# Kernel optimization log

Hardware: AMD Instinct MI355X
Metric: run time of the kernel (lower is better)

Reference implementation:

```python
import jax, jax.numpy as jnp
import numpy as np

B, N, E, K = 4, 40000, 240000, 128
C_IN, C_W, C_OUT, N_BLOCK = 6, 128, 3, 4


def setup_inputs() -> dict:
    key = jax.random.key(0)
    ks = jax.random.split(key, 20)
    s = lambda k, sh, fan: jax.random.normal(k, sh, jnp.float32) / np.sqrt(fan).astype(np.float32)
    inp = {}
    inp["x_in"] = jax.random.normal(ks[0], (B, N, C_IN), jnp.float32)
    inp["mass"] = jax.random.uniform(ks[1], (B, N), jnp.float32) + 0.1  # positive lumped mass
    inp["evals"] = jax.random.uniform(ks[2], (B, K), jnp.float32) * 10.0  # nonneg Laplacian eigenvalues
    inp["evecs"] = jax.random.normal(ks[3], (B, N, K), jnp.float32) / np.float32(np.sqrt(N))
    inp["rows"] = jax.random.randint(ks[4], (E,), 0, N, jnp.int32)
    inp["cols"] = jax.random.randint(ks[5], (E,), 0, N, jnp.int32)
    inp["gradX_vals"] = jax.random.normal(ks[6], (B, E), jnp.float32)
    inp["gradY_vals"] = jax.random.normal(ks[7], (B, E), jnp.float32)
    inp["w_first"] = s(ks[8], (C_IN, C_W), C_IN)
    inp["b_first"] = jnp.zeros((C_W,), jnp.float32)
    inp["diff_time"] = jax.random.uniform(ks[9], (N_BLOCK, C_W), jnp.float32) * 0.1 + 1e-4  # learned times, clamped positive
    inp["A_re"] = s(ks[10], (N_BLOCK, C_W, C_W), C_W)
    inp["A_im"] = s(ks[11], (N_BLOCK, C_W, C_W), C_W)
    inp["mlp_w0"] = s(ks[12], (N_BLOCK, 3 * C_W, C_W), 3 * C_W)
    inp["mlp_b0"] = jnp.zeros((N_BLOCK, C_W), jnp.float32)
    inp["mlp_w1"] = s(ks[13], (N_BLOCK, C_W, C_W), C_W)
    inp["mlp_b1"] = jnp.zeros((N_BLOCK, C_W), jnp.float32)
    inp["mlp_w2"] = s(ks[14], (N_BLOCK, C_W, C_W), C_W)
    inp["mlp_b2"] = jnp.zeros((N_BLOCK, C_W), jnp.float32)
    inp["w_last"] = s(ks[15], (C_W, C_OUT), C_W)
    inp["b_last"] = jnp.zeros((C_OUT,), jnp.float32)
    return inp


def reference(x_in, mass, evals, evecs, rows, cols, gradX_vals, gradY_vals,
              w_first, b_first, diff_time, A_re, A_im,
              mlp_w0, mlp_b0, mlp_w1, mlp_b1, mlp_w2, mlp_b2, w_last, b_last):
    def spmm(vals, x):
        # sparse [N,N] COO (shared pattern, per-sample vals) @ dense [N,C]
        return jax.ops.segment_sum(vals[:, None] * x[cols], rows, num_segments=N)

    x = x_in @ w_first + b_first  # [B,N,C_W]
    for i in range(N_BLOCK):
        # --- LearnedTimeDiffusion (spectral) ---
        x_spec = jnp.einsum('bnk,bnc->bkc', evecs, x * mass[..., None])  # [B,K,C]
        coefs = jnp.exp(-evals[:, :, None] * diff_time[i][None, None, :])  # [B,K,C]
        x_diffuse = jnp.einsum('bnk,bkc->bnc', evecs, coefs * x_spec)  # [B,N,C]
        # --- per-sample sparse gradient operators (the batched torch.mm loop) ---
        gX = jax.vmap(spmm)(gradX_vals, x_diffuse)  # [B,N,C]
        gY = jax.vmap(spmm)(gradY_vals, x_diffuse)  # [B,N,C]
        # --- SpatialGradientFeatures with learned rotations (complex multiply) ---
        Breal = gX @ A_re[i] - gY @ A_im[i]
        Bimag = gY @ A_re[i] + gX @ A_im[i]
        grad_feat = jnp.tanh(gX * Breal + gY * Bimag)  # [B,N,C]
        # --- MiniMLP + residual ---
        feat = jnp.concatenate([x, x_diffuse, grad_feat], axis=-1)  # [B,N,3C]
        h = jax.nn.relu(feat @ mlp_w0[i] + mlp_b0[i])
        h = jax.nn.relu(h @ mlp_w1[i] + mlp_b1[i])
        h = h @ mlp_w2[i] + mlp_b2[i]
        x = h + x
    return x @ w_last + b_last  # [B,N,C_OUT]
```

## Files before the change

### kernel.cpp

```cpp
#include <hip/hip_runtime.h>

#define B_ 4
#define N_ 40000
#define E_ 240000
#define NB_SCAN ((N_ + 255) / 256)

typedef unsigned short u16;
typedef unsigned int u32;
typedef __attribute__((ext_vector_type(8))) short bf16x8;
typedef __attribute__((ext_vector_type(4))) float f32x4;

__device__ __forceinline__ float b2f(u16 h) {
    u32 u = ((u32)h) << 16;
    return __uint_as_float(u);
}
__device__ __forceinline__ u16 f2b(float f) {
    u32 u = __float_as_uint(f);
    u32 r = (u + 0x7fffu + ((u >> 16) & 1u)) >> 16;
    return (u16)r;
}

__global__ __launch_bounds__(256) void first_linear_kern(
    const float* __restrict__ x_in, const float* __restrict__ w,
    const float* __restrict__ bias, u16* __restrict__ xout, int M)
{
    __shared__ float sw[6 * 128];
    __shared__ float sb[128];
    int t = threadIdx.x;
    for (int i = t; i < 768; i += 256) sw[i] = w[i];
    if (t < 128) sb[t] = bias[t];
    __syncthreads();
    int idx = blockIdx.x * 256 + t;
    int row = idx >> 4;
    int cg = (idx & 15) * 8;
    if (row >= M) return;
    const float* xr = x_in + (size_t)row * 6;
    float xv[6];
#pragma unroll
    for (int j = 0; j < 6; j++) xv[j] = xr[j];
    float acc[8];
#pragma unroll
    for (int i = 0; i < 8; i++) acc[i] = sb[cg + i];
#pragma unroll
    for (int j = 0; j < 6; j++)
#pragma unroll
        for (int i = 0; i < 8; i++) acc[i] += xv[j] * sw[j * 128 + cg + i];
    ushort4 h0, h1;
    h0.x = f2b(acc[0]); h0.y = f2b(acc[1]); h0.z = f2b(acc[2]); h0.w = f2b(acc[3]);
    h1.x = f2b(acc[4]); h1.y = f2b(acc[5]); h1.z = f2b(acc[6]); h1.w = f2b(acc[7]);
    uint4 pk;
    pk.x = (u32)h0.x | ((u32)h0.y << 16);
    pk.y = (u32)h0.z | ((u32)h0.w << 16);
    pk.z = (u32)h1.x | ((u32)h1.y << 16);
    pk.w = (u32)h1.z | ((u32)h1.w << 16);
    *(uint4*)(xout + (size_t)row * 128 + cg) = pk;
}

__global__ __launch_bounds__(256) void pack_w_kern(
    const float* __restrict__ src, u16* __restrict__ dst, int K)
{
    int i = blockIdx.z;
    src += (size_t)i * K * 128;
    dst += (size_t)i * K * 128;
    int idx = blockIdx.x * 256 + threadIdx.x;
    int n = idx / K;
    int k = idx % K;
    dst[idx] = f2b(src[(size_t)k * 128 + n]);
}

__global__ __launch_bounds__(256) void pack_rot_kern(
    const float* __restrict__ Are, const float* __restrict__ Aim,
    u16* __restrict__ WR1, u16* __restrict__ WR2)
{
    int i = blockIdx.z;
    const float* are = Are + (size_t)i * 16384;
    const float* aim = Aim + (size_t)i * 16384;
    int idx = blockIdx.x * 256 + threadIdx.x;
    int n = idx >> 8;
    int k = idx & 255;
    float v1, v2;
    if (k < 128) { float a = are[(size_t)k * 128 + n]; v1 = a; v2 = a; }
    else         { float a = aim[(size_t)(k - 128) * 128 + n]; v1 = -a; v2 = a; }
    WR1[(size_t)i * 32768 + idx] = f2b(v1);
    WR2[(size_t)i * 32768 + idx] = f2b(v2);
}

__global__ __launch_bounds__(256) void hist_kern(const int* __restrict__ rows, int* count)
{
    int e = blockIdx.x * 256 + threadIdx.x;
    if (e < E_) atomicAdd(&count[rows[e]], 1);
}

__device__ __forceinline__ int block_incl_scan_256(int v, int t)
{
    __shared__ int wsum[4];
    int lane = t & 63;
    int wid = t >> 6;
    int x = v;
#pragma unroll
    for (int off = 1; off < 64; off <<= 1) {
        int y = __shfl_up(x, off);
        if (lane >= off) x += y;
    }
    if (lane == 63) wsum[wid] = x;
    __syncthreads();
    if (t == 0) {
        int s = 0;
#pragma unroll
        for (int i = 0; i < 4; i++) { int tm = wsum[i]; wsum[i] = s; s += tm; }
    }
    __syncthreads();
    return x + wsum[wid];
}

__global__ __launch_bounds__(256) void scan1_kern(
    const int* __restrict__ count, int* __restrict__ excl_out,
    int* __restrict__ blockTotals)
{
    int t = threadIdx.x;
    int g = blockIdx.x * 256 + t;
    int v = (g < N_) ? count[g] : 0;
    int incl = block_incl_scan_256(v, t);
    if (g < N_) excl_out[g] = incl - v;
    if (t == 255) blockTotals[blockIdx.x] = incl;
}

__global__ __launch_bounds__(256) void scan2_kern(
    const int* __restrict__ blockTotals, int* __restrict__ blockOffs,
    int* __restrict__ totalOut)
{
    int t = threadIdx.x;
    int v = (t < NB_SCAN) ? blockTotals[t] : 0;
    int incl = block_incl_scan_256(v, t);
    if (t < NB_SCAN) blockOffs[t] = incl - v;
    if (t == 255) *totalOut = incl;
}

__global__ __launch_bounds__(256) void scan3_kern(
    int* __restrict__ rowptr, int* __restrict__ nextp,
    const int* __restrict__ blockOffs)
{
    int t = threadIdx.x;
    int g = blockIdx.x * 256 + t;
    if (g >= N_) return;
    int v = rowptr[g] + blockOffs[blockIdx.x];
    rowptr[g] = v;
    nextp[g] = v;
}

__global__ __launch_bounds__(256) void scatter_idx_kern(
    const int* __restrict__ rows, const int* __restrict__ cols,
    int* nextp, int* __restrict__ scols, int* __restrict__ sperm)
{
    int e = blockIdx.x * 256 + threadIdx.x;
    if (e >= E_) return;
    int r = rows[e];
    int pos = atomicAdd(&nextp[r], 1);
    scols[pos] = cols[e];
    sperm[pos] = e;
}

__global__ __launch_bounds__(256) void gather_vals_kern(
    const int* __restrict__ sperm,
    const float* __restrict__ gvx, const float* __restrict__ gvy,
    float* __restrict__ svx, float* __restrict__ svy)
{
    int pos = blockIdx.x * 256 + threadIdx.x;
    if (pos >= E_) return;
    int e = sperm[pos];
#pragma unroll
    for (int b = 0; b < B_; b++) {
        svx[(size_t)b * E_ + pos] = gvx[(size_t)b * E_ + e];
        svy[(size_t)b * E_ + pos] = gvy[(size_t)b * E_ + e];
    }
}

__global__ __launch_bounds__(256) void spmm_csr_kern(
    const int* __restrict__ rowptr, const int* __restrict__ scols,
    const float* __restrict__ svx, const float* __restrict__ svy,
    const u16* __restrict__ xd_b, u16* __restrict__ gXh, u16* __restrict__ gYh)
{
    int t = threadIdx.x;
    int r = blockIdx.x * 4 + (t >> 6);
    int c2 = (t & 63) * 2;
    int beg = rowptr[r], end = rowptr[r + 1];
    float ax0 = 0.f, ax1 = 0.f, ay0 = 0.f, ay1 = 0.f;
    int j = beg;
    for (; j + 1 < end; j += 2) {
        int ca = scols[j], cb = scols[j + 1];
        u32 xwa = *(const u32*)(xd_b + (size_t)ca * 128 + c2);
        u32 xwb = *(const u32*)(xd_b + (size_t)cb * 128 + c2);
        float vxa = svx[j], vya = svy[j];
        float vxb = svx[j + 1], vyb = svy[j + 1];
        float xa0 = b2f((u16)(xwa & 0xffffu)), xa1 = b2f((u16)(xwa >> 16));
        float xb0 = b2f((u16)(xwb & 0xffffu)), xb1 = b2f((u16)(xwb >> 16));
        ax0 += vxa * xa0; ax1 += vxa * xa1;
        ay0 += vya * xa0; ay1 += vya * xa1;
        ax0 += vxb * xb0; ax1 += vxb * xb1;
        ay0 += vyb * xb0; ay1 += vyb * xb1;
    }
    if (j < end) {
        int col = scols[j];
        u32 xw = *(const u32*)(xd_b + (size_t)col * 128 + c2);
        float x0 = b2f((u16)(xw & 0xffffu));
        float x1 = b2f((u16)(xw >> 16));
        float vx = svx[j], vy = svy[j];
        ax0 += vx * x0; ax1 += vx * x1;
        ay0 += vy * x0; ay1 += vy * x1;
    }
    u32 px = (u32)f2b(ax0) | ((u32)f2b(ax1) << 16);
    u32 py = (u32)f2b(ay0) | ((u32)f2b(ay1) << 16);
    *(u32*)(gXh + (size_t)r * 128 + c2) = px;
    *(u32*)(gYh + (size_t)r * 128 + c2) = py;
}

__global__ __launch_bounds__(256) void spec_stage1_mfma_kern(
    const u16* __restrict__ x, const float* __restrict__ mass,
    const float* __restrict__ evecs, float* __restrict__ partials)
{
    __shared__ __align__(16) u16 sEVh[128][40];
    __shared__ __align__(16) u16 sEVl[128][40];
    __shared__ __align__(16) u16 sXM[128][40];
    int b = blockIdx.y;
    int pb = blockIdx.x;
    const u16* xb = x + (size_t)b * N_ * 128;
    const float* mb = mass + (size_t)b * N_;
    const float* eb = evecs + (size_t)b * N_ * 128;
    float* dst = partials + ((size_t)b * 128 + pb) * 16384;

    int t = threadIdx.x;
    int wv = t >> 6;
    int lane = t & 63;
    int quad = lane >> 4;
    int r16 = lane & 15;
    int kb = wv * 32;
    int kc = (t & 63) * 2;
    int nh = wv;

    f32x4 acc[2][8];
#pragma unroll
    for (int i = 0; i < 2; i++)
#pragma unroll
        for (int j = 0; j < 8; j++) acc[i][j] = (f32x4){0.f, 0.f, 0.f, 0.f};

    for (int ch = pb; ch < N_ / 32; ch += 128) {
        int nbase = ch * 32 + nh * 8;
        float4 m0 = *(const float4*)(mb + nbase);
        float4 m1 = *(const float4*)(mb + nbase + 4);
        float mm[8] = {m0.x, m0.y, m0.z, m0.w, m1.x, m1.y, m1.z, m1.w};
        u32 eh0[4], eh1[4], el0[4], el1[4], xq0[4], xq1[4];
#pragma unroll
        for (int jp = 0; jp < 4; jp++) {
            eh0[jp] = 0; eh1[jp] = 0; el0[jp] = 0;
            el1[jp] = 0; xq0[jp] = 0; xq1[jp] = 0;
        }
#pragma unroll
        for (int j = 0; j < 8; j++) {
            float2 e = *(const float2*)(eb + (size_t)(nbase + j) * 128 + kc);
            u32 xw = *(const u32*)(xb + (size_t)(nbase + j) * 128 + kc);
            u16 h0 = f2b(e.x);
            u16 h1 = f2b(e.y);
            u16 l0 = f2b(e.x - b2f(h0));
            u16 l1 = f2b(e.y - b2f(h1));
            u16 q0 = f2b(b2f((u16)(xw & 0xffffu)) * mm[j]);
            u16 q1 = f2b(b2f((u16)(xw >> 16)) * mm[j]);
            int sh = (j & 1) * 16;
            int jp = j >> 1;
            eh0[jp] |= ((u32)h0) << sh; eh1[jp] |= ((u32)h1) << sh;
            el0[jp] |= ((u32)l0) << sh; el1[jp] |= ((u32)l1) << sh;
            xq0[jp] |= ((u32)q0) << sh; xq1[jp] |= ((u32)q1) << sh;
        }
        __syncthreads();
        *(uint4*)&sEVh[kc][nh * 8]     = make_uint4(eh0[0], eh0[1], eh0[2], eh0[3]);
        *(uint4*)&sEVh[kc + 1][nh * 8] = make_uint4(eh1[0], eh1[1], eh1[2], eh1[3]);
        *(uint4*)&sEVl[kc][nh * 8]     = make_uint4(el0[0], el0[1], el0[2], el0[3]);
        *(uint4*)&sEVl[kc + 1][nh * 8] = make_uint4(el1[0], el1[1], el1[2], el1[3]);
        *(uint4*)&sXM[kc][nh * 8]      = make_uint4(xq0[0], xq0[1], xq0[2], xq0[3]);
        *(uint4*)&sXM[kc + 1][nh * 8]  = make_uint4(xq1[0], xq1[1], xq1[2], xq1[3]);
        __syncthreads();

        bf16x8 ah0 = *(const bf16x8*)&sEVh[kb + r16][quad * 8];
        bf16x8 ah1 = *(const bf16x8*)&sEVh[kb + 16 + r16][quad * 8];
        bf16x8 al0 = *(const bf16x8*)&sEVl[kb + r16][quad * 8];
        bf16x8 al1 = *(const bf16x8*)&sEVl[kb + 16 + r16][quad * 8];
#pragma unroll
        for (int nt = 0; nt < 8; nt++) {
            bf16x8 bx = *(const bf16x8*)&sXM[nt * 16 + r16][quad * 8];
            acc[0][nt] = __builtin_amdgcn_mfma_f32_16x16x32_bf16(ah0, bx, acc[0][nt], 0, 0, 0);
            acc[1][nt] = __builtin_amdgcn_mfma_f32_16x16x32_bf16(ah1, bx, acc[1][nt], 0, 0, 0);
            acc[0][nt] = __builtin_amdgcn_mfma_f32_16x16x32_bf16(al0, bx, acc[0][nt], 0, 0, 0);
            acc[1][nt] = __builtin_amdgcn_mfma_f32_16x16x32_bf16(al1, bx, acc[1][nt], 0, 0, 0);
        }
    }

#pragma unroll
    for (int mt = 0; mt < 2; mt++)
#pragma unroll
        for (int nt = 0; nt < 8; nt++)
#pragma unroll
            for (int reg = 0; reg < 4; reg++) {
                int kk = kb + mt * 16 + quad * 4 + reg;
                int cc = nt * 16 + r16;
                dst[(size_t)kk * 128 + cc] = acc[mt][nt][reg];
            }
}

__global__ __launch_bounds__(128) void spec_stage2_coef_kern(
    const float* __restrict__ partials, const float* __restrict__ evals,
    const float* __restrict__ dt, u16* __restrict__ ys_t)
{
    int b = blockIdx.x >> 7;
    int k = blockIdx.x & 127;
    int c = threadIdx.x;
    const float* p = partials + (size_t)b * 128 * 16384 + (size_t)k * 128 + c;
    float s = 0.f;
#pragma unroll 8
    for (int pb = 0; pb < 128; pb++) s += p[(size_t)pb * 16384];
    float co = expf(-evals[b * 128 + k] * dt[c]);
    ys_t[((size_t)b * 128 + c) * 128 + k] = f2b(s * co);
}

template <int KK, bool AF32>
__global__ __launch_bounds__(256) void mgemm_kern(
    const void* __restrict__ A0v,
    const u16* __restrict__ Wp, u16* __restrict__ outp,
    size_t aBatch, size_t wBatch, size_t oBatch)
{
    __shared__ u16 sA[64][72];
    __shared__ u16 sB[128][72];
    int z = blockIdx.z;
    const u16* Wb = Wp + wBatch * (size_t)z;
    size_t aOff = aBatch * (size_t)z;
    size_t oOff = oBatch * (size_t)z;

    int t = threadIdx.x;
    int m0 = blockIdx.x * 64;
    int wv = t >> 6;
    int lane = t & 63;
    int quad = lane >> 4;
    int r16 = lane & 15;
    int mw = (wv & 1) * 32;
    int nw = (wv >> 1) * 64;

    f32x4 acc[2][4];
#pragma unroll
    for (int i = 0; i < 2; i++)
#pragma unroll
        for (int j = 0; j < 4; j++) acc[i][j] = (f32x4){0.f, 0.f, 0.f, 0.f};

#pragma unroll 1
    for (int kt = 0; kt < KK / 64; kt++) {
        int kbase = kt * 64;
        __syncthreads();
        if (AF32) {
            const float* Af = (const float*)A0v + aOff;
#pragma unroll
            for (int p = 0; p < 4; p++) {
                int idx = p * 256 + t;
                int row = idx >> 4;
                int seg = idx & 15;
                float4 v = *(const float4*)(Af + (size_t)(m0 + row) * 128 + kbase + seg * 4);
                ushort4 h;
                h.x = f2b(v.x); h.y = f2b(v.y); h.z = f2b(v.z); h.w = f2b(v.w);
                *(ushort4*)&sA[row][seg * 4] = h;
            }
        } else {
            const u16* Ah = (const u16*)A0v + aOff;
#pragma unroll
            for (int p = 0; p < 2; p++) {
                int idx = p * 256 + t;
                int row = idx >> 3;
                int seg = idx & 7;
                *(uint4*)&sA[row][seg * 8] =
                    *(const uint4*)(Ah + (size_t)(m0 + row) * 128 + kbase + seg * 8);
            }
        }
        {
#pragma unroll
            for (int p = 0; p < 4; p++) {
                int idx = p * 256 + t;
                int n = idx >> 3;
                int seg = idx & 7;
                *(uint4*)&sB[n][seg * 8] =
                    *(const uint4*)(Wb + (size_t)n * KK + kbase + seg * 8);
            }
        }
        __syncthreads();

#pragma unroll
        for (int ks = 0; ks < 2; ks++) {
            int ko = ks * 32 + quad * 8;
            bf16x8 a0 = *(const bf16x8*)&sA[mw + r16][ko];
            bf16x8 a1 = *(const bf16x8*)&sA[mw + 16 + r16][ko];
            bf16x8 b0 = *(const bf16x8*)&sB[nw + r16][ko];
            bf16x8 b1 = *(const bf16x8*)&sB[nw + 16 + r16][ko];
            bf16x8 b2 = *(const bf16x8*)&sB[nw + 32 + r16][ko];
            bf16x8 b3 = *(const bf16x8*)&sB[nw + 48 + r16][ko];
            acc[0][0] = __builtin_amdgcn_mfma_f32_16x16x32_bf16(a0, b0, acc[0][0], 0, 0, 0);
            acc[0][1] = __builtin_amdgcn_mfma_f32_16x16x32_bf16(a0, b1, acc[0][1], 0, 0, 0);
            acc[0][2] = __builtin_amdgcn_mfma_f32_16x16x32_bf16(a0, b2, acc[0][2], 0, 0, 0);
            acc[0][3] = __builtin_amdgcn_mfma_f32_16x16x32_bf16(a0, b3, acc[0][3], 0, 0, 0);
            acc[1][0] = __builtin_amdgcn_mfma_f32_16x16x32_bf16(a1, b0, acc[1][0], 0, 0, 0);
            acc[1][1] = __builtin_amdgcn_mfma_f32_16x16x32_bf16(a1, b1, acc[1][1], 0, 0, 0);
            acc[1][2] = __builtin_amdgcn_mfma_f32_16x16x32_bf16(a1, b2, acc[1][2], 0, 0, 0);
            acc[1][3] = __builtin_amdgcn_mfma_f32_16x16x32_bf16(a1, b3, acc[1][3], 0, 0, 0);
        }
    }

#pragma unroll
    for (int nt = 0; nt < 4; nt++) {
        int col = nw + nt * 16 + r16;
#pragma unroll
        for (int mt = 0; mt < 2; mt++) {
#pragma unroll
            for (int reg = 0; reg < 4; reg++) {
                int row = m0 + mw + mt * 16 + quad * 4 + reg;
                outp[oOff + (size_t)row * 128 + col] = f2b(acc[mt][nt][reg]);
            }
        }
    }
}

__global__ __launch_bounds__(256) void mlp_rot_fused_kern(
    const u16* __restrict__ xg, const u16* __restrict__ xdg,
    const u16* __restrict__ gXY,
    const u16* __restrict__ WR1, const u16* __restrict__ WR2,
    const u16* __restrict__ W0, const u16* __restrict__ W1, const u16* __restrict__ W2,
    const float* __restrict__ b0, const float* __restrict__ b1, const float* __restrict__ b2,
    int batch0, u16* __restrict__ outp)
{
    __shared__ u16 sGX[64][136];
    __shared__ u16 sGY[64][136];
    __shared__ u16 sB[128][72];
    __shared__ __align__(16) u16 sHbuf[9728];
    __shared__ u16 sA[64][72];
#define HV(r, c) sHbuf[(r) * 152 + (c)]
#define WV(n, c) sHbuf[(n) * 72 + (c)]

    const size_t NZ = (size_t)N_ * 128;
    int z = blockIdx.z;
    int batch = batch0 + z;
    const u16* gX = gXY + (size_t)z * 2 * NZ;
    const u16* gY = gX + NZ;
    int m0n = blockIdx.x * 64;
    size_t growBase = ((size_t)batch * N_ + m0n) * 128;

    int t = threadIdx.x;
    int wv = t >> 6;
    int lane = t & 63;
    int quad = lane >> 4;
    int r16 = lane & 15;
    int mw = (wv & 1) * 32;
    int nw = (wv >> 1) * 64;

#pragma unroll
    for (int p = 0; p < 4; p++) {
        int idx = p * 256 + t;
        int row = idx >> 4;
        int seg = idx & 15;
        *(uint4*)&sGX[row][seg * 8] = *(const uint4*)(gX + (size_t)(m0n + row) * 128 + seg * 8);
        *(uint4*)&sGY[row][seg * 8] = *(const uint4*)(gY + (size_t)(m0n + row) * 128 + seg * 8);
    }

    f32x4 accRe[2][4], accIm[2][4];
#pragma unroll
    for (int i = 0; i < 2; i++)
#pragma unroll
        for (int j = 0; j < 4; j++) {
            accRe[i][j] = (f32x4){0.f, 0.f, 0.f, 0.f};
            accIm[i][j] = (f32x4){0.f, 0.f, 0.f, 0.f};
        }

#pragma unroll 1
    for (int c = 0; c < 4; c++) {
        __syncthreads();
#pragma unroll
        for (int p = 0; p < 4; p++) {
            int idx = p * 256 + t;
            int n = idx >> 3;
            int seg = idx & 7;
            *(uint4*)&sB[n][seg * 8] = *(const uint4*)(WR1 + (size_t)n * 256 + c * 64 + seg * 8);
            *(uint4*)&WV(n, seg * 8) = *(const uint4*)(WR2 + (size_t)n * 256 + c * 64 + seg * 8);
        }
        __syncthreads();

        const u16 (*sRe)[136] = (c < 2) ? sGX : sGY;
        const u16 (*sIm)[136] = (c < 2) ? sGY : sGX;
        int kob = (c & 1) * 64;
#pragma unroll
        for (int ks = 0; ks < 2; ks++) {
            int ko = kob + ks * 32 + quad * 8;
            int kb = ks * 32 + quad * 8;
            bf16x8 aRe0 = *(const bf16x8*)&sRe[mw + r16][ko];
            bf16x8 aRe1 = *(const bf16x8*)&sRe[mw + 16 + r16][ko];
            bf16x8 aIm0 = *(const bf16x8*)&sIm[mw + r16][ko];
            bf16x8 aIm1 = *(const bf16x8*)&sIm[mw + 16 + r16][ko];
#pragma unroll
            for (int j = 0; j < 4; j++) {
                bf16x8 w1f = *(const bf16x8*)&sB[nw + 16 * j + r16][kb];
                bf16x8 w2f = *(const bf16x8*)&WV(nw + 16 * j + r16, kb);
                accRe[0][j] = __builtin_amdgcn_mfma_f32_16x16x32_bf16(aRe0, w1f, accRe[0][j], 0, 0, 0);
                accRe[1][j] = __builtin_amdgcn_mfma_f32_16x16x32_bf16(aRe1, w1f, accRe[1][j], 0, 0, 0);
                accIm[0][j] = __builtin_amdgcn_mfma_f32_16x16x32_bf16(aIm0, w2f, accIm[0][j], 0, 0, 0);
                accIm[1][j] = __builtin_amdgcn_mfma_f32_16x16x32_bf16(aIm1, w2f, accIm[1][j], 0, 0, 0);
            }
        }
    }

    __syncthreads();
#pragma unroll
    for (int nt = 0; nt < 4; nt++) {
        int col = nw + nt * 16 + r16;
#pragma unroll
        for (int mt = 0; mt < 2; mt++)
#pragma unroll
            for (int reg = 0; reg < 4; reg++) {
                int lrow = mw + mt * 16 + quad * 4 + reg;
                float gx = b2f(sGX[lrow][col]);
                float gy = b2f(sGY[lrow][col]);
                float v = tanhf(gx * accRe[mt][nt][reg] + gy * accIm[mt][nt][reg]);
                sGX[lrow][col] = f2b(v);
            }
    }

    f32x4 acc[2][4];
#pragma unroll
    for (int i = 0; i < 2; i++)
#pragma unroll
        for (int j = 0; j < 4; j++) acc[i][j] = (f32x4){0.f, 0.f, 0.f, 0.f};
#pragma unroll 1
    for (int kt = 0; kt < 6; kt++) {
        int kbase = kt * 64;
        int kloc = kbase & 127;
        __syncthreads();
        if (kt < 4) {
            const u16* Ap = (kt < 2) ? xg : xdg;
#pragma unroll
            for (int p = 0; p < 2; p++) {
                int idx = p * 256 + t;
                int row = idx >> 3;
                int seg = idx & 7;
                *(uint4*)&sA[row][seg * 8] =
                    *(const uint4*)(Ap + growBase + (size_t)row * 128 + kloc + seg * 8);
            }
        }
#pragma unroll
        for (int p = 0; p < 4; p++) {
            int idx = p * 256 + t;
            int n = idx >> 3;
            int seg = idx & 7;
            *(uint4*)&sB[n][seg * 8] = *(const uint4*)(W0 + (size_t)n * 384 + kbase + seg * 8);
        }
        __syncthreads();
#pragma unroll
        for (int ks = 0; ks < 2; ks++) {
            int ko = ks * 32 + quad * 8;
            bf16x8 a0, a1;
            if (kt < 4) {
                a0 = *(const bf16x8*)&sA[mw + r16][ko];
                a1 = *(const bf16x8*)&sA[mw + 16 + r16][ko];
            } else {
                a0 = *(const bf16x8*)&sGX[mw + r16][kloc + ko];
                a1 = *(const bf16x8*)&sGX[mw + 16 + r16][kloc + ko];
            }
#pragma unroll
            for (int j = 0; j < 4; j++) {
                bf16x8 bj = *(const bf16x8*)&sB[nw + 16 * j + r16][ko];
                acc[0][j] = __builtin_amdgcn_mfma_f32_16x16x32_bf16(a0, bj, acc[0][j], 0, 0, 0);
                acc[1][j] = __builtin_amdgcn_mfma_f32_16x16x32_bf16(a1, bj, acc[1][j], 0, 0, 0);
            }
        }
    }
    __syncthreads();
#pragma unroll
    for (int nt = 0; nt < 4; nt++) {
        int col = nw + nt * 16 + r16;
        float bv = b0[col];
#pragma unroll
        for (int mt = 0; mt < 2; mt++)
#pragma unroll
            for (int reg = 0; reg < 4; reg++) {
                int rl = mw + mt * 16 + quad * 4 + reg;
                HV(rl, col) = f2b(fmaxf(acc[mt][nt][reg] + bv, 0.f));
            }
    }

#pragma unroll
    for (int i = 0; i < 2; i++)
#pragma unroll
        for (int j = 0; j < 4; j++) acc[i][j] = (f32x4){0.f, 0.f, 0.f, 0.f};
#pragma unroll 1
    for (int kt = 0; kt < 2; kt++) {
        int kbase = kt * 64;
        __syncthreads();
#pragma unroll
        for (int p = 0; p < 4; p++) {
            int idx = p * 256 + t;
            int n = idx >> 3;
            int seg = idx & 7;
            *(uint4*)&sB[n][seg * 8] = *(const uint4*)(W1 + (size_t)n * 128 + kbase + seg * 8);
        }
        __syncthreads();
#pragma unroll
        for (int ks = 0; ks < 2; ks++) {
            int ko = kbase + ks * 32 + quad * 8;
            int kb = ks * 32 + quad * 8;
            bf16x8 a0 = *(const bf16x8*)&HV(mw + r16, ko);
            bf16x8 a1 = *(const bf16x8*)&HV(mw + 16 + r16, ko);
#pragma unroll
            for (int j = 0; j < 4; j++) {
                bf16x8 bj = *(const bf16x8*)&sB[nw + 16 * j + r16][kb];
                acc[0][j] = __builtin_amdgcn_mfma_f32_16x16x32_bf16(a0, bj, acc[0][j], 0, 0, 0);
                acc[1][j] = __builtin_amdgcn_mfma_f32_16x16x32_bf16(a1, bj, acc[1][j], 0, 0, 0);
            }
        }
    }
    __syncthreads();
#pragma unroll
    for (int nt = 0; nt < 4; nt++) {
        int col = nw + nt * 16 + r16;
        float bv = b1[col];
#pragma unroll
        for (int mt = 0; mt < 2; mt++)
#pragma unroll
            for (int reg = 0; reg < 4; reg++) {
                int rl = mw + mt * 16 + quad * 4 + reg;
                HV(rl, col) = f2b(fmaxf(acc[mt][nt][reg] + bv, 0.f));
            }
    }

#pragma unroll
    for (int i = 0; i < 2; i++)
#pragma unroll
        for (int j = 0; j < 4; j++) acc[i][j] = (f32x4){0.f, 0.f, 0.f, 0.f};
#pragma unroll 1
    for (int kt = 0; kt < 2; kt++) {
        int kbase = kt * 64;
        __syncthreads();
#pragma unroll
        for (int p = 0; p < 4; p++) {
            int idx = p * 256 + t;
            int n = idx >> 3;
            int seg = idx & 7;
            *(uint4*)&sB[n][seg * 8] = *(const uint4*)(W2 + (size_t)n * 128 + kbase + seg * 8);
        }
        __syncthreads();
#pragma unroll
        for (int ks = 0; ks < 2; ks++) {
            int ko = kbase + ks * 32 + quad * 8;
            int kb = ks * 32 + quad * 8;
            bf16x8 a0 = *(const bf16x8*)&HV(mw + r16, ko);
            bf16x8 a1 = *(const bf16x8*)&HV(mw + 16 + r16, ko);
#pragma unroll
            for (int j = 0; j < 4; j++) {
                bf16x8 bj = *(const bf16x8*)&sB[nw + 16 * j + r16][kb];
                acc[0][j] = __builtin_amdgcn_mfma_f32_16x16x32_bf16(a0, bj, acc[0][j], 0, 0, 0);
                acc[1][j] = __builtin_amdgcn_mfma_f32_16x16x32_bf16(a1, bj, acc[1][j], 0, 0, 0);
            }
        }
    }
#pragma unroll
    for (int nt = 0; nt < 4; nt++) {
        int col = nw + nt * 16 + r16;
        float bv = b2[col];
#pragma unroll
        for (int mt = 0; mt < 2; mt++)
#pragma unroll
            for (int reg = 0; reg < 4; reg++) {
                int row = mw + mt * 16 + quad * 4 + reg;
                float v = acc[mt][nt][reg] + bv + b2f(xg[growBase + (size_t)row * 128 + col]);
                outp[growBase + (size_t)row * 128 + col] = f2b(v);
            }
    }
#undef HV
#undef WV
}

__global__ __launch_bounds__(256) void last_linear_kern(
    const u16* __restrict__ x, const float* __restrict__ w,
    const float* __restrict__ bias, float* __restrict__ outp, int M)
{
    __shared__ float sw[128 * 3];
    int t = threadIdx.x;
    for (int i = t; i < 384; i += 256) sw[i] = w[i];
    __syncthreads();
    int wave = t >> 6;
    int lane = t & 63;
    int row = blockIdx.x * 4 + wave;
    if (row >= M) return;
    const u16* xr = x + (size_t)row * 128;
    float p0 = 0.f, p1 = 0.f, p2 = 0.f;
#pragma unroll
    for (int h = 0; h < 2; h++) {
        int c = lane + h * 64;
        float xv = b2f(xr[c]);
        p0 += xv * sw[c * 3 + 0];
        p1 += xv * sw[c * 3 + 1];
        p2 += xv * sw[c * 3 + 2];
    }
#pragma unroll
    for (int off = 32; off > 0; off >>= 1) {
        p0 += __shfl_xor(p0, off);
        p1 += __shfl_xor(p1, off);
        p2 += __shfl_xor(p2, off);
    }
    if (lane == 0) {
        float* o = outp + (size_t)row * 3;
        o[0] = p0 + bias[0];
        o[1] = p1 + bias[1];
        o[2] = p2 + bias[2];
    }
}

extern "C" void kernel_launch(void* const* d_in, const int* in_sizes, int n_in,
                              void* d_out, int out_size, void* d_ws, size_t ws_size,
                              hipStream_t stream)
{
    const float* x_in    = (const float*)d_in[0];
    const float* mass    = (const float*)d_in[1];
    const float* evals   = (const float*)d_in[2];
    const float* evecs   = (const float*)d_in[3];
    const int*   rows    = (const int*)  d_in[4];
    const int*   cols    = (const int*)  d_in[5];
    const float* gvx     = (const float*)d_in[6];
    const float* gvy     = (const float*)d_in[7];
    const float* w_first = (const float*)d_in[8];
    const float* b_first = (const float*)d_in[9];
    const float* dtimes  = (const float*)d_in[10];
    const float* A_re    = (const float*)d_in[11];
    const float* A_im    = (const float*)d_in[12];
    const float* w0      = (const float*)d_in[13];
    const float* b0      = (const float*)d_in[14];
    const float* w1      = (const float*)d_in[15];
    const float* b1      = (const float*)d_in[16];
    const float* w2      = (const float*)d_in[17];
    const float* b2      = (const float*)d_in[18];
    const float* w_last  = (const float*)d_in[19];
    const float* b_last  = (const float*)d_in[20];
    float* outp = (float*)d_out;

    const size_t SZ = (size_t)B_ * N_ * 128;
    const size_t NZ = (size_t)N_ * 128;

    u16* P0 = (u16*)d_ws;
    u16* P1 = P0 + SZ;
    u16* GF = P1 + SZ;
    float* SC = (float*)(GF + SZ);
    u16* ys_t = (u16*)(SC + 8388608);
    u16* WP0 = (u16*)(SC + 2 * NZ);
    u16* WP1 = WP0 + 4 * 49152;
    u16* WP2 = WP1 + 4 * 16384;
    u16* WR1 = WP2 + 4 * 16384;
    u16* WR2 = WR1 + 4 * 32768;
    int* rowptr = (int*)(WR2 + 4 * 32768);
    int* nextp  = rowptr + 40004;
    int* scols  = nextp + N_;
    float* svx  = (float*)(scols + E_);
    float* svy  = svx + (size_t)B_ * E_;

    u16* x  = P0;
    u16* xd = P1;
    const int M = B_ * N_;

    int* bTot  = (int*)SC;
    int* bOff  = bTot + 512;
    int* sperm = bTot + 1024;
    hipMemsetAsync(nextp, 0, N_ * sizeof(int), stream);
    hist_kern<<<dim3((E_ + 255) / 256), 256, 0, stream>>>(rows, nextp);
    scan1_kern<<<dim3(NB_SCAN), 256, 0, stream>>>(nextp, rowptr, bTot);
    scan2_kern<<<dim3(1), 256, 0, stream>>>(bTot, bOff, rowptr + N_);
    scan3_kern<<<dim3(NB_SCAN), 256, 0, stream>>>(rowptr, nextp, bOff);
    scatter_idx_kern<<<dim3((E_ + 255) / 256), 256, 0, stream>>>(
        rows, cols, nextp, scols, sperm);
    gather_vals_kern<<<dim3((E_ + 255) / 256), 256, 0, stream>>>(
        sperm, gvx, gvy, svx, svy);

    pack_w_kern<<<dim3(192, 1, 4), 256, 0, stream>>>(w0, WP0, 384);
    pack_w_kern<<<dim3(64, 1, 4), 256, 0, stream>>>(w1, WP1, 128);
    pack_w_kern<<<dim3(64, 1, 4), 256, 0, stream>>>(w2, WP2, 128);
    pack_rot_kern<<<dim3(128, 1, 4), 256, 0, stream>>>(A_re, A_im, WR1, WR2);

    first_linear_kern<<<dim3(M * 16 / 256), 256, 0, stream>>>(x_in, w_first, b_first, x, M);

    u16* GXY = GF;

    for (int i = 0; i < 4; i++) {
        spec_stage1_mfma_kern<<<dim3(128, B_), 256, 0, stream>>>(x, mass, evecs, SC);
        spec_stage2_coef_kern<<<dim3(B_ * 128), 128, 0, stream>>>(
            SC, evals, dtimes + (size_t)i * 128, ys_t);
        mgemm_kern<128, true><<<dim3(N_ / 64, 1, B_), 256, 0, stream>>>(
            evecs, ys_t, xd, NZ, (size_t)128 * 128, NZ);
        for (int p = 0; p < 2; p++) {
            for (int zz = 0; zz < 2; zz++) {
                int b = p * 2 + zz;
                spmm_csr_kern<<<dim3(N_ / 4), 256, 0, stream>>>(
                    rowptr, scols, svx + (size_t)b * E_, svy + (size_t)b * E_,
                    xd + (size_t)b * NZ,
                    GXY + (size_t)zz * 2 * NZ, GXY + (size_t)zz * 2 * NZ + NZ);
            }
            mlp_rot_fused_kern<<<dim3(N_ / 64, 1, 2), 256, 0, stream>>>(
                x, xd, GXY,
                WR1 + (size_t)i * 32768, WR2 + (size_t)i * 32768,
                WP0 + (size_t)i * 49152, WP1 + (size_t)i * 16384, WP2 + (size_t)i * 16384,
                b0 + (size_t)i * 128, b1 + (size_t)i * 128, b2 + (size_t)i * 128,
                p * 2, xd);
        }
        u16* tmp = x; x = xd; xd = tmp;
    }

    last_linear_kern<<<dim3(M / 4), 256, 0, stream>>>(x, w_last, b_last, outp, M);
}
```

Before: 1.366 ms.

## Batch SpMM and fused MLP launches over all samples, widen MLP blocks to 512 threads

The two-pass loop that ran SpMM and the fused rotation+MLP kernel on two samples at a time is replaced by single launches covering all four samples through blockIdx.z. The extra gradient storage this needs comes from reusing the spectral partials buffer (SC) as a second GXY buffer. The MLP kernel now runs 8 waves per block, each computing a 32x32 output tile instead of 32x64, with global-to-shared load loops reshaped to match. The aim is fewer launches, better GPU fill and more latency hiding. The risks are that SC may not be large enough to hold two samples' gradients, and that the narrower per-wave tiles re-read A fragments from shared memory more often.

```diff
diff --git a/kernel.cpp b/kernel.cpp
--- a/kernel.cpp
+++ b/kernel.cpp
@@ -178,8 +178,17 @@
 __global__ __launch_bounds__(256) void spmm_csr_kern(
     const int* __restrict__ rowptr, const int* __restrict__ scols,
     const float* __restrict__ svx, const float* __restrict__ svy,
-    const u16* __restrict__ xd_b, u16* __restrict__ gXh, u16* __restrict__ gYh)
-{
+    const u16* __restrict__ xd, u16* __restrict__ gXY0, u16* __restrict__ gXY1)
+{
+    const size_t NZ = (size_t)N_ * 128;
+    int z = blockIdx.z;
+    const float* svx_b = svx + (size_t)z * E_;
+    const float* svy_b = svy + (size_t)z * E_;
+    const u16* xd_b = xd + (size_t)z * NZ;
+    u16* base = (z < 2) ? (gXY0 + (size_t)z * 2 * NZ) : (gXY1 + (size_t)(z - 2) * 2 * NZ);
+    u16* gXh = base;
+    u16* gYh = base + NZ;
+
     int t = threadIdx.x;
     int r = blockIdx.x * 4 + (t >> 6);
     int c2 = (t & 63) * 2;
@@ -190,8 +199,8 @@
         int ca = scols[j], cb = scols[j + 1];
         u32 xwa = *(const u32*)(xd_b + (size_t)ca * 128 + c2);
         u32 xwb = *(const u32*)(xd_b + (size_t)cb * 128 + c2);
-        float vxa = svx[j], vya = svy[j];
-        float vxb = svx[j + 1], vyb = svy[j + 1];
+        float vxa = svx_b[j], vya = svy_b[j];
+        float vxb = svx_b[j + 1], vyb = svy_b[j + 1];
         float xa0 = b2f((u16)(xwa & 0xffffu)), xa1 = b2f((u16)(xwa >> 16));
         float xb0 = b2f((u16)(xwb & 0xffffu)), xb1 = b2f((u16)(xwb >> 16));
         ax0 += vxa * xa0; ax1 += vxa * xa1;
@@ -204,7 +213,7 @@
         u32 xw = *(const u32*)(xd_b + (size_t)col * 128 + c2);
         float x0 = b2f((u16)(xw & 0xffffu));
         float x1 = b2f((u16)(xw >> 16));
-        float vx = svx[j], vy = svy[j];
+        float vx = svx_b[j], vy = svy_b[j];
         ax0 += vx * x0; ax1 += vx * x1;
         ay0 += vy * x0; ay1 += vy * x1;
     }
@@ -421,13 +430,13 @@
     }
 }
 
-__global__ __launch_bounds__(256) void mlp_rot_fused_kern(
+__global__ __launch_bounds__(512) void mlp_rot_fused_kern(
     const u16* __restrict__ xg, const u16* __restrict__ xdg,
-    const u16* __restrict__ gXY,
+    const u16* __restrict__ gXY0, const u16* __restrict__ gXY1,
     const u16* __restrict__ WR1, const u16* __restrict__ WR2,
     const u16* __restrict__ W0, const u16* __restrict__ W1, const u16* __restrict__ W2,
     const float* __restrict__ b0, const float* __restrict__ b1, const float* __restrict__ b2,
-    int batch0, u16* __restrict__ outp)
+    u16* __restrict__ outp)
 {
     __shared__ u16 sGX[64][136];
     __shared__ u16 sGY[64][136];
@@ -439,11 +448,10 @@
 
     const size_t NZ = (size_t)N_ * 128;
     int z = blockIdx.z;
-    int batch = batch0 + z;
-    const u16* gX = gXY + (size_t)z * 2 * NZ;
+    const u16* gX = (z < 2) ? (gXY0 + (size_t)z * 2 * NZ) : (gXY1 + (size_t)(z - 2) * 2 * NZ);
     const u16* gY = gX + NZ;
     int m0n = blockIdx.x * 64;
-    size_t growBase = ((size_t)batch * N_ + m0n) * 128;
+    size_t growBase = ((size_t)z * N_ + m0n) * 128;
 
     int t = threadIdx.x;
     int wv = t >> 6;
@@ -451,22 +459,22 @@
     int quad = lane >> 4;
     int r16 = lane & 15;
     int mw = (wv & 1) * 32;
-    int nw = (wv >> 1) * 64;
-
-#pragma unroll
-    for (int p = 0; p < 4; p++) {
-        int idx = p * 256 + t;
+    int nw = (wv >> 1) * 32;
+
+#pragma unroll
+    for (int p = 0; p < 2; p++) {
+        int idx = p * 512 + t;
         int row = idx >> 4;
         int seg = idx & 15;
         *(uint4*)&sGX[row][seg * 8] = *(const uint4*)(gX + (size_t)(m0n + row) * 128 + seg * 8);
         *(uint4*)&sGY[row][seg * 8] = *(const uint4*)(gY + (size_t)(m0n + row) * 128 + seg * 8);
     }
 
-    f32x4 accRe[2][4], accIm[2][4];
+    f32x4 accRe[2][2], accIm[2][2];
 #pragma unroll
     for (int i = 0; i < 2; i++)
 #pragma unroll
-        for (int j = 0; j < 4; j++) {
+        for (int j = 0; j < 2; j++) {
             accRe[i][j] = (f32x4){0.f, 0.f, 0.f, 0.f};
             accIm[i][j] = (f32x4){0.f, 0.f, 0.f, 0.f};
         }
@@ -475,8 +483,8 @@
     for (int c = 0; c < 4; c++) {
         __syncthreads();
 #pragma unroll
-        for (int p = 0; p < 4; p++) {
-            int idx = p * 256 + t;
+        for (int p = 0; p < 2; p++) {
+            int idx = p * 512 + t;
             int n = idx >> 3;
             int seg = idx & 7;
             *(uint4*)&sB[n][seg * 8] = *(const uint4*)(WR1 + (size_t)n * 256 + c * 64 + seg * 8);
@@ -496,7 +504,7 @@
             bf16x8 aIm0 = *(const bf16x8*)&sIm[mw + r16][ko];
             bf16x8 aIm1 = *(const bf16x8*)&sIm[mw + 16 + r16][ko];
 #pragma unroll
-            for (int j = 0; j < 4; j++) {
+            for (int j = 0; j < 2; j++) {
                 bf16x8 w1f = *(const bf16x8*)&sB[nw + 16 * j + r16][kb];
                 bf16x8 w2f = *(const bf16x8*)&WV(nw + 16 * j + r16, kb);
                 accRe[0][j] = __builtin_amdgcn_mfma_f32_16x16x32_bf16(aRe0, w1f, accRe[0][j], 0, 0, 0);
@@ -509,7 +517,7 @@
 
     __syncthreads();
 #pragma unroll
-    for (int nt = 0; nt < 4; nt++) {
+    for (int nt = 0; nt < 2; nt++) {
         int col = nw + nt * 16 + r16;
 #pragma unroll
         for (int mt = 0; mt < 2; mt++)
@@ -523,11 +531,11 @@
             }
     }
 
-    f32x4 acc[2][4];
+    f32x4 acc[2][2];
 #pragma unroll
     for (int i = 0; i < 2; i++)
 #pragma unroll
-        for (int j = 0; j < 4; j++) acc[i][j] = (f32x4){0.f, 0.f, 0.f, 0.f};
+        for (int j = 0; j < 2; j++) acc[i][j] = (f32x4){0.f, 0.f, 0.f, 0.f};
 #pragma unroll 1
     for (int kt = 0; kt < 6; kt++) {
         int kbase = kt * 64;
@@ -535,18 +543,16 @@
         __syncthreads();
         if (kt < 4) {
             const u16* Ap = (kt < 2) ? xg : xdg;
-#pragma unroll
-            for (int p = 0; p < 2; p++) {
-                int idx = p * 256 + t;
-                int row = idx >> 3;
-                int seg = idx & 7;
+            {
+                int row = t >> 3;
+                int seg = t & 7;
                 *(uint4*)&sA[row][seg * 8] =
                     *(const uint4*)(Ap + growBase + (size_t)row * 128 + kloc + seg * 8);
             }
         }
 #pragma unroll
-        for (int p = 0; p < 4; p++) {
-            int idx = p * 256 + t;
+        for (int p = 0; p < 2; p++) {
+            int idx = p * 512 + t;
             int n = idx >> 3;
             int seg = idx & 7;
             *(uint4*)&sB[n][seg * 8] = *(const uint4*)(W0 + (size_t)n * 384 + kbase + seg * 8);
@@ -564,7 +570,7 @@
                 a1 = *(const bf16x8*)&sGX[mw + 16 + r16][kloc + ko];
             }
 #pragma unroll
-            for (int j = 0; j < 4; j++) {
+            for (int j = 0; j < 2; j++) {
                 bf16x8 bj = *(const bf16x8*)&sB[nw + 16 * j + r16][ko];
                 acc[0][j] = __builtin_amdgcn_mfma_f32_16x16x32_bf16(a0, bj, acc[0][j], 0, 0, 0);
                 acc[1][j] = __builtin_amdgcn_mfma_f32_16x16x32_bf16(a1, bj, acc[1][j], 0, 0, 0);
@@ -573,7 +579,7 @@
     }
     __syncthreads();
 #pragma unroll
-    for (int nt = 0; nt < 4; nt++) {
+    for (int nt = 0; nt < 2; nt++) {
         int col = nw + nt * 16 + r16;
         float bv = b0[col];
 #pragma unroll
@@ -588,14 +594,14 @@
 #pragma unroll
     for (int i = 0; i < 2; i++)
 #pragma unroll
-        for (int j = 0; j < 4; j++) acc[i][j] = (f32x4){0.f, 0.f, 0.f, 0.f};
+        for (int j = 0; j < 2; j++) acc[i][j] = (f32x4){0.f, 0.f, 0.f, 0.f};
 #pragma unroll 1
     for (int kt = 0; kt < 2; kt++) {
         int kbase = kt * 64;
         __syncthreads();
 #pragma unroll
-        for (int p = 0; p < 4; p++) {
-            int idx = p * 256 + t;
+        for (int p = 0; p < 2; p++) {
+            int idx = p * 512 + t;
             int n = idx >> 3;
             int seg = idx & 7;
             *(uint4*)&sB[n][seg * 8] = *(const uint4*)(W1 + (size_t)n * 128 + kbase + seg * 8);
@@ -608,7 +614,7 @@
             bf16x8 a0 = *(const bf16x8*)&HV(mw + r16, ko);
             bf16x8 a1 = *(const bf16x8*)&HV(mw + 16 + r16, ko);
 #pragma unroll
-            for (int j = 0; j < 4; j++) {
+            for (int j = 0; j < 2; j++) {
                 bf16x8 bj = *(const bf16x8*)&sB[nw + 16 * j + r16][kb];
                 acc[0][j] = __builtin_amdgcn_mfma_f32_16x16x32_bf16(a0, bj, acc[0][j], 0, 0, 0);
                 acc[1][j] = __builtin_amdgcn_mfma_f32_16x16x32_bf16(a1, bj, acc[1][j], 0, 0, 0);
@@ -617,7 +623,7 @@
     }
     __syncthreads();
 #pragma unroll
-    for (int nt = 0; nt < 4; nt++) {
+    for (int nt = 0; nt < 2; nt++) {
         int col = nw + nt * 16 + r16;
         float bv = b1[col];
 #pragma unroll
@@ -632,14 +638,14 @@
 #pragma unroll
     for (int i = 0; i < 2; i++)
 #pragma unroll
-        for (int j = 0; j < 4; j++) acc[i][j] = (f32x4){0.f, 0.f, 0.f, 0.f};
+        for (int j = 0; j < 2; j++) acc[i][j] = (f32x4){0.f, 0.f, 0.f, 0.f};
 #pragma unroll 1
     for (int kt = 0; kt < 2; kt++) {
         int kbase = kt * 64;
         __syncthreads();
 #pragma unroll
-        for (int p = 0; p < 4; p++) {
-            int idx = p * 256 + t;
+        for (int p = 0; p < 2; p++) {
+            int idx = p * 512 + t;
             int n = idx >> 3;
             int seg = idx & 7;
             *(uint4*)&sB[n][seg * 8] = *(const uint4*)(W2 + (size_t)n * 128 + kbase + seg * 8);
@@ -652,7 +658,7 @@
             bf16x8 a0 = *(const bf16x8*)&HV(mw + r16, ko);
             bf16x8 a1 = *(const bf16x8*)&HV(mw + 16 + r16, ko);
 #pragma unroll
-            for (int j = 0; j < 4; j++) {
+            for (int j = 0; j < 2; j++) {
                 bf16x8 bj = *(const bf16x8*)&sB[nw + 16 * j + r16][kb];
                 acc[0][j] = __builtin_amdgcn_mfma_f32_16x16x32_bf16(a0, bj, acc[0][j], 0, 0, 0);
                 acc[1][j] = __builtin_amdgcn_mfma_f32_16x16x32_bf16(a1, bj, acc[1][j], 0, 0, 0);
@@ -660,7 +666,7 @@
         }
     }
 #pragma unroll
-    for (int nt = 0; nt < 4; nt++) {
+    for (int nt = 0; nt < 2; nt++) {
         int col = nw + nt * 16 + r16;
         float bv = b2[col];
 #pragma unroll
@@ -782,7 +788,8 @@
 
     first_linear_kern<<<dim3(M * 16 / 256), 256, 0, stream>>>(x_in, w_first, b_first, x, M);
 
-    u16* GXY = GF;
+    u16* GXY0 = GF;
+    u16* GXY1 = (u16*)SC;
 
     for (int i = 0; i < 4; i++) {
         spec_stage1_mfma_kern<<<dim3(128, B_), 256, 0, stream>>>(x, mass, evecs, SC);
@@ -790,21 +797,14 @@
             SC, evals, dtimes + (size_t)i * 128, ys_t);
         mgemm_kern<128, true><<<dim3(N_ / 64, 1, B_), 256, 0, stream>>>(
             evecs, ys_t, xd, NZ, (size_t)128 * 128, NZ);
-        for (int p = 0; p < 2; p++) {
-            for (int zz = 0; zz < 2; zz++) {
-                int b = p * 2 + zz;
-                spmm_csr_kern<<<dim3(N_ / 4), 256, 0, stream>>>(
-                    rowptr, scols, svx + (size_t)b * E_, svy + (size_t)b * E_,
-                    xd + (size_t)b * NZ,
-                    GXY + (size_t)zz * 2 * NZ, GXY + (size_t)zz * 2 * NZ + NZ);
-            }
-            mlp_rot_fused_kern<<<dim3(N_ / 64, 1, 2), 256, 0, stream>>>(
-                x, xd, GXY,
-                WR1 + (size_t)i * 32768, WR2 + (size_t)i * 32768,
-                WP0 + (size_t)i * 49152, WP1 + (size_t)i * 16384, WP2 + (size_t)i * 16384,
-                b0 + (size_t)i * 128, b1 + (size_t)i * 128, b2 + (size_t)i * 128,
-                p * 2, xd);
-        }
+        spmm_csr_kern<<<dim3(N_ / 4, 1, B_), 256, 0, stream>>>(
+            rowptr, scols, svx, svy, xd, GXY0, GXY1);
+        mlp_rot_fused_kern<<<dim3(N_ / 64, 1, B_), 512, 0, stream>>>(
+            x, xd, GXY0, GXY1,
+            WR1 + (size_t)i * 32768, WR2 + (size_t)i * 32768,
+            WP0 + (size_t)i * 49152, WP1 + (size_t)i * 16384, WP2 + (size_t)i * 16384,
+            b0 + (size_t)i * 128, b1 + (size_t)i * 128, b2 + (size_t)i * 128,
+            xd);
         u16* tmp = x; x = xd; xd = tmp;
     }
 
```

Result: faster. 1.209 ms, median of 2 (-11.5%).
